# Kernel tuning notes

Measured on AMD Instinct MI355X. Metric: run time of the kernel, lower is better.

Reference implementation:

```python
import jax, jax.numpy as jnp
import numpy as np

N_NODES = 50000
N_EDGES = 600000
N_GRAPHS = 64
D_FEAT = 128
DIM_H = 128
N_HOPS = 3
OUT_DIM = 10


def setup_inputs() -> dict:
    key = jax.random.key(0)
    ks = jax.random.split(key, 16)
    x = jax.random.normal(ks[0], (N_NODES, D_FEAT), dtype=jnp.float32)
    edge_index = jax.random.randint(ks[1], (2, N_EDGES), 0, N_NODES, dtype=jnp.int64)
    batch = jnp.sort(jax.random.randint(ks[2], (N_NODES,), 0, N_GRAPHS, dtype=jnp.int64))
    def glorot(k, shape):
        fan = shape[0] + shape[1]
        return jax.random.uniform(k, shape, jnp.float32, -1.0, 1.0) * np.sqrt(6.0 / fan)
    # GCNConv weights stored as [in, out]; Linear weights stored as [in, out]
    W1 = glorot(ks[3], (D_FEAT, DIM_H)); b1 = jnp.zeros((DIM_H,), jnp.float32)
    W2 = glorot(ks[4], (DIM_H, DIM_H)); b2 = jnp.zeros((DIM_H,), jnp.float32)
    W3 = glorot(ks[5], (DIM_H, DIM_H)); b3 = jnp.zeros((DIM_H,), jnp.float32)
    H3 = DIM_H * N_HOPS
    lin1_W = glorot(ks[6], (H3, H3)); lin1_b = jnp.zeros((H3,), jnp.float32)
    lin2_W = glorot(ks[7], (H3, OUT_DIM)); lin2_b = jnp.zeros((OUT_DIM,), jnp.float32)
    return {"x": x, "W1": W1, "b1": b1, "W2": W2, "b2": b2, "W3": W3, "b3": b3,
            "lin1_W": lin1_W, "lin1_b": lin1_b, "lin2_W": lin2_W, "lin2_b": lin2_b,
            "edge_index": edge_index, "batch": batch}


def gcn_conv(x, W, b, src, dst, n_nodes):
    # PyG GCNConv (add_self_loops=True, normalize=True):
    #   deg[i] = in-degree at target + 1 (self loop); norm = d^-1/2[src] * d^-1/2[dst]
    deg = jnp.zeros((n_nodes,), x.dtype).at[dst].add(1.0) + 1.0
    dinv = jax.lax.rsqrt(deg)
    xw = x @ W  # [N, H] transform before propagate
    coef = (dinv[src] * dinv[dst])[:, None]
    agg = jnp.zeros_like(xw).at[dst].add(xw[src] * coef)
    agg = agg + xw * (dinv * dinv)[:, None]  # self-loop messages
    return agg + b


def global_mean_pool(h, batch, n_graphs):
    sums = jax.ops.segment_sum(h, batch, num_segments=n_graphs)
    cnt = jax.ops.segment_sum(jnp.ones((h.shape[0],), h.dtype), batch, num_segments=n_graphs)
    return sums / jnp.maximum(cnt, 1.0)[:, None]


def reference(x, W1, b1, W2, b2, W3, b3, lin1_W, lin1_b, lin2_W, lin2_b, edge_index, batch):
    src, dst = edge_index[0], edge_index[1]
    n = x.shape[0]
    h1 = gcn_conv(x, W1, b1, src, dst, n)
    h2 = gcn_conv(h1, W2, b2, src, dst, n)
    h3 = gcn_conv(h2, W3, b3, src, dst, n)
    pooled = jnp.concatenate([global_mean_pool(h, batch, N_GRAPHS) for h in (h1, h2, h3)], axis=1)
    h = jax.nn.relu(pooled @ lin1_W + lin1_b)
    # dropout is identity in eval mode
    h = h @ lin2_W + lin2_b
    return (h, jax.nn.log_softmax(h, axis=1))
```

## Files before the change

### kernel.cpp

```cpp
#include <hip/hip_runtime.h>
#include <hip/hip_fp16.h>
#include <math.h>

#define N_NODES 50000
#define N_EDGES 600000
#define N_GRAPHS 64
#define DFEAT 128
#define H3 384
#define OUTD 10
#define SCAN_BLOCKS 196
#define FILL_BLOCKS 2344
#define POOL_CHUNKS 16
#define APAD 136

typedef _Float16 f16x8 __attribute__((ext_vector_type(8)));
typedef float f32x4 __attribute__((ext_vector_type(4)));
typedef float f32x2 __attribute__((ext_vector_type(2)));

__global__ __launch_bounds__(256) void k_deg(const int* __restrict__ ei, int* __restrict__ deg,
                                             int* __restrict__ rank) {
    int e = blockIdx.x * 256 + threadIdx.x;
    if (e >= N_EDGES) return;
    int dst = ei[N_EDGES + e];
    rank[e] = atomicAdd(&deg[dst], 1);
}

__global__ __launch_bounds__(256) void k_part(const int* __restrict__ deg, int* __restrict__ part) {
    __shared__ int red[256];
    int tid = threadIdx.x;
    int i = blockIdx.x * 256 + tid;
    red[tid] = (i < N_NODES) ? deg[i] : 0;
    __syncthreads();
    for (int s = 128; s > 0; s >>= 1) {
        if (tid < s) red[tid] += red[tid + s];
        __syncthreads();
    }
    if (tid == 0) part[blockIdx.x] = red[0];
}

__global__ __launch_bounds__(256) void k_scanpart(const int* __restrict__ part, int* __restrict__ base) {
    __shared__ int buf[256];
    int tid = threadIdx.x;
    int v = (tid < SCAN_BLOCKS) ? part[tid] : 0;
    buf[tid] = v;
    __syncthreads();
    for (int d = 1; d < 256; d <<= 1) {
        int t = (tid >= d) ? buf[tid - d] : 0;
        __syncthreads();
        buf[tid] += t;
        __syncthreads();
    }
    if (tid < SCAN_BLOCKS) base[tid] = buf[tid] - v;
}

__global__ __launch_bounds__(256) void k_offsets(const int* __restrict__ deg, const int* __restrict__ base,
                                                 int* __restrict__ offs, float* __restrict__ dinv) {
    __shared__ int buf[256];
    int tid = threadIdx.x;
    int i = blockIdx.x * 256 + tid;
    int v = (i < N_NODES) ? deg[i] : 0;
    buf[tid] = v;
    __syncthreads();
    for (int d = 1; d < 256; d <<= 1) {
        int t = (tid >= d) ? buf[tid - d] : 0;
        __syncthreads();
        buf[tid] += t;
        __syncthreads();
    }
    if (i < N_NODES) {
        int excl = base[blockIdx.x] + buf[tid] - v;
        offs[i] = excl;
        dinv[i] = rsqrtf((float)v + 1.0f);
        if (i == N_NODES - 1) offs[N_NODES] = base[blockIdx.x] + buf[tid];
    }
}

__global__ __launch_bounds__(256) void k_fill_prep(const int* __restrict__ ei, const int* __restrict__ offs,
                                                   const int* __restrict__ rank, const float* __restrict__ dinv,
                                                   unsigned int* __restrict__ epack,
                                                   const float* __restrict__ W1, const float* __restrict__ W2,
                                                   const float* __restrict__ W3, _Float16* __restrict__ Wt,
                                                   float* __restrict__ pooled) {
    int b = blockIdx.x;
    if (b < FILL_BLOCKS) {
        int e = b * 256 + threadIdx.x;
        if (e >= N_EDGES) return;
        int s = ei[e];
        int t = ei[N_EDGES + e];
        unsigned short dh = __half_as_ushort(__float2half(dinv[s]));
        epack[offs[t] + rank[e]] = (unsigned int)s | ((unsigned int)dh << 16);
    } else if (b < FILL_BLOCKS + 192) {
        int idx = (b - FILL_BLOCKS) * 256 + threadIdx.x;
        int l = idx >> 14, r = idx & 16383;
        const float* W = (l == 0) ? W1 : (l == 1) ? W2 : W3;
        int k = r >> 7, n = r & 127;
        Wt[l * 16384 + n * 128 + k] = (_Float16)W[k * 128 + n];
    } else {
        int idx = (b - FILL_BLOCKS - 192) * 256 + threadIdx.x;
        if (idx < N_GRAPHS * H3) pooled[idx] = 0.0f;
    }
}

template <bool A_FP16>
__global__ __launch_bounds__(256) void gemm_mfma(const void* __restrict__ Aptr, const _Float16* __restrict__ Wt,
                                                 unsigned char* __restrict__ T, int M) {
    __shared__ _Float16 Ws[128 * APAD];
    int tid = threadIdx.x;
    int base = blockIdx.x * 64;
    for (int c = tid; c < 2048; c += 256) {
        int n = c >> 4, c8 = (c & 15) << 3;
        *(f16x8*)&Ws[n * APAD + c8] = *(const f16x8*)&Wt[n * 128 + c8];
    }
    int wave = tid >> 6, lane = tid & 63;
    int m = lane & 15, quad = lane >> 4;
    int gr = base + wave * 16 + m;
    int grc = (gr < M) ? gr : (M - 1);
    f16x8 areg[4];
    if (A_FP16) {
        const _Float16* A = (const _Float16*)Aptr;
#pragma unroll
        for (int kc = 0; kc < 4; ++kc)
            areg[kc] = *(const f16x8*)&A[(size_t)grc * 128 + kc * 32 + quad * 8];
    } else {
        const float* A = (const float*)Aptr;
#pragma unroll
        for (int kc = 0; kc < 4; ++kc) {
            const float* src = A + (size_t)grc * 128 + kc * 32 + quad * 8;
            float4 v0 = *(const float4*)(src);
            float4 v1 = *(const float4*)(src + 4);
            f16x8 h;
            h[0] = (_Float16)v0.x; h[1] = (_Float16)v0.y; h[2] = (_Float16)v0.z; h[3] = (_Float16)v0.w;
            h[4] = (_Float16)v1.x; h[5] = (_Float16)v1.y; h[6] = (_Float16)v1.z; h[7] = (_Float16)v1.w;
            areg[kc] = h;
        }
    }
    __syncthreads();
    f32x4 acc[8];
#pragma unroll
    for (int ct = 0; ct < 8; ++ct) acc[ct] = (f32x4){0.f, 0.f, 0.f, 0.f};
#pragma unroll
    for (int kc = 0; kc < 4; ++kc) {
#pragma unroll
        for (int ct = 0; ct < 8; ++ct) {
            f16x8 b = *(const f16x8*)&Ws[(ct * 16 + m) * APAD + kc * 32 + quad * 8];
            acc[ct] = __builtin_amdgcn_mfma_f32_16x16x32_f16(b, areg[kc], acc[ct], 0, 0, 0);
        }
    }
    if (gr < M) {
#pragma unroll
        for (int ct = 0; ct < 8; ++ct) {
            int col = ct * 16 + quad * 4;
            int p = __builtin_amdgcn_cvt_pk_fp8_f32(acc[ct][0], acc[ct][1], 0, false);
            p     = __builtin_amdgcn_cvt_pk_fp8_f32(acc[ct][2], acc[ct][3], p, true);
            *(int*)(T + (size_t)gr * 128 + col) = p;
        }
    }
}

__global__ __launch_bounds__(256) void gather_agg(const unsigned int* __restrict__ T32,
                                                  const unsigned int* __restrict__ epack,
                                                  const int* __restrict__ offs,
                                                  const float* __restrict__ dinv, const float* __restrict__ bias,
                                                  __half2* __restrict__ H2) {
    int h = threadIdx.x >> 5;
    int l32 = threadIdx.x & 31;
    int node = blockIdx.x * 8 + h;
    unsigned su = T32[(size_t)node * 32 + l32];
    float di = dinv[node];
    float4 b4 = *(const float4*)(bias + l32 * 4);
    float a0 = 0.f, a1 = 0.f, a2 = 0.f, a3 = 0.f;
    int lo = offs[node], hi = offs[node + 1];
    int hm1 = hi - 1;
    for (int e0 = lo; e0 < hi; e0 += 16) {
        unsigned p[16];
#pragma unroll
        for (int j = 0; j < 16; ++j) p[j] = epack[min(e0 + j, hm1)];
        unsigned u[16];
#pragma unroll
        for (int j = 0; j < 16; ++j) u[j] = T32[(size_t)(p[j] & 0xffffu) * 32 + l32];
#pragma unroll
        for (int j = 0; j < 16; ++j) {
            float c = (e0 + j < hi) ? __half2float(__ushort_as_half((unsigned short)(p[j] >> 16))) : 0.0f;
            f32x2 tl = __builtin_amdgcn_cvt_pk_f32_fp8(u[j], false);
            f32x2 th = __builtin_amdgcn_cvt_pk_f32_fp8(u[j], true);
            a0 += tl.x * c; a1 += tl.y * c; a2 += th.x * c; a3 += th.y * c;
        }
    }
    f32x2 sl = __builtin_amdgcn_cvt_pk_f32_fp8(su, false), sh = __builtin_amdgcn_cvt_pk_f32_fp8(su, true);
    float dd = di * di;
    float r0 = di * a0 + sl.x * dd + b4.x;
    float r1 = di * a1 + sl.y * dd + b4.y;
    float r2 = di * a2 + sh.x * dd + b4.z;
    float r3 = di * a3 + sh.y * dd + b4.w;
    H2[(size_t)node * 64 + l32 * 2]     = __floats2half2_rn(r0, r1);
    H2[(size_t)node * 64 + l32 * 2 + 1] = __floats2half2_rn(r2, r3);
}

__global__ __launch_bounds__(256) void pool_kernel(const __half2* __restrict__ H0,
                                                   const __half2* __restrict__ H1,
                                                   const __half2* __restrict__ H2buf,
                                                   const int* __restrict__ batch,
                                                   float* __restrict__ pooled) {
    __shared__ int bounds[2];
    __shared__ float2 red[256];
    int g = blockIdx.x >> 4;
    int chunk = blockIdx.x & (POOL_CHUNKS - 1);
    int tid = threadIdx.x;
    int d2 = tid & 63, sub = tid >> 6;
    if (tid < 2) {
        int target = g + tid;
        int lo = 0, hi = N_NODES;
        while (lo < hi) {
            int mid = (lo + hi) >> 1;
            if (batch[mid] < target) lo = mid + 1; else hi = mid;
        }
        bounds[tid] = lo;
    }
    __syncthreads();
    int lo = bounds[0], hi = bounds[1];
    int n = hi - lo;
    int per = (n + POOL_CHUNKS - 1) / POOL_CHUNKS;
    int s = lo + chunk * per;
    int e = s + per; if (e > hi) e = hi;
    const __half2* Hs[3] = {H0, H1, H2buf};
    for (int l = 0; l < 3; ++l) {
        const __half2* H = Hs[l];
        float ax = 0.0f, ay = 0.0f;
        for (int r = s + sub; r < e; r += 4) {
            float2 v = __half22float2(H[(size_t)r * 64 + d2]);
            ax += v.x; ay += v.y;
        }
        red[tid] = make_float2(ax, ay);
        __syncthreads();
        if (sub == 0 && s < e) {
            float2 v0 = red[d2], v1 = red[64 + d2], v2 = red[128 + d2], v3 = red[192 + d2];
            atomicAdd(&pooled[g * H3 + l * 128 + d2 * 2],     v0.x + v1.x + v2.x + v3.x);
            atomicAdd(&pooled[g * H3 + l * 128 + d2 * 2 + 1], v0.y + v1.y + v2.y + v3.y);
        }
        __syncthreads();
    }
}

__global__ __launch_bounds__(384) void mlp_kernel(const float* __restrict__ pooled,
                                                  const int* __restrict__ batch,
                                                  const float* __restrict__ l1W, const float* __restrict__ l1b,
                                                  const float* __restrict__ l2W, const float* __restrict__ l2b,
                                                  float* __restrict__ out) {
    __shared__ float p[H3];
    __shared__ float hid[H3];
    __shared__ float o10[OUTD];
    __shared__ int bnd[2];
    int g = blockIdx.x, tid = threadIdx.x;
    if (tid < 2) {
        int target = g + tid;
        int lo = 0, hi = N_NODES;
        while (lo < hi) {
            int mid = (lo + hi) >> 1;
            if (batch[mid] < target) lo = mid + 1; else hi = mid;
        }
        bnd[tid] = lo;
    }
    __syncthreads();
    float inv = 1.0f / fmaxf((float)(bnd[1] - bnd[0]), 1.0f);
    p[tid] = pooled[g * H3 + tid] * inv;
    __syncthreads();
    float acc = l1b[tid];
    for (int k = 0; k < H3; ++k) acc += p[k] * l1W[k * H3 + tid];
    hid[tid] = fmaxf(acc, 0.0f);
    __syncthreads();
    if (tid < OUTD) {
        float o = l2b[tid];
        for (int k = 0; k < H3; ++k) o += hid[k] * l2W[k * OUTD + tid];
        o10[tid] = o;
        out[g * OUTD + tid] = o;
    }
    __syncthreads();
    if (tid == 0) {
        float m = o10[0];
        for (int j = 1; j < OUTD; ++j) m = fmaxf(m, o10[j]);
        float s = 0.0f;
        for (int j = 0; j < OUTD; ++j) s += expf(o10[j] - m);
        float lse = m + logf(s);
        for (int j = 0; j < OUTD; ++j) out[N_GRAPHS * OUTD + g * OUTD + j] = o10[j] - lse;
    }
}

extern "C" void kernel_launch(void* const* d_in, const int* in_sizes, int n_in,
                              void* d_out, int out_size, void* d_ws, size_t ws_size,
                              hipStream_t stream) {
    const float* x      = (const float*)d_in[0];
    const float* W1     = (const float*)d_in[1];
    const float* b1     = (const float*)d_in[2];
    const float* W2     = (const float*)d_in[3];
    const float* b2     = (const float*)d_in[4];
    const float* W3     = (const float*)d_in[5];
    const float* b3     = (const float*)d_in[6];
    const float* lin1_W = (const float*)d_in[7];
    const float* lin1_b = (const float*)d_in[8];
    const float* lin2_W = (const float*)d_in[9];
    const float* lin2_b = (const float*)d_in[10];
    const int* edge_index = (const int*)d_in[11];
    const int* batch      = (const int*)d_in[12];

    char* ws = (char*)d_ws;
    auto alloc = [&](size_t bytes) -> void* {
        void* p = (void*)ws;
        ws += (bytes + 255) & ~(size_t)255;
        return p;
    };
    int*   deg    = (int*)  alloc((size_t)N_NODES * 4);
    int*   part   = (int*)  alloc((size_t)SCAN_BLOCKS * 4);
    int*   pbase  = (int*)  alloc((size_t)SCAN_BLOCKS * 4);
    int*   offs   = (int*)  alloc((size_t)(N_NODES + 1) * 4);
    int*   rank   = (int*)  alloc((size_t)N_EDGES * 4);
    float* dinv   = (float*)alloc((size_t)N_NODES * 4);
    unsigned int* epack = (unsigned int*)alloc((size_t)N_EDGES * 4);
    unsigned char* T = (unsigned char*)alloc((size_t)N_NODES * 128);
    __half* Hbuf[3];
    for (int l = 0; l < 3; ++l) Hbuf[l] = (__half*)alloc((size_t)N_NODES * 128 * 2);
    _Float16* Wt  = (_Float16*)alloc((size_t)3 * 128 * 128 * 2);
    float* pooled = (float*)alloc((size_t)N_GRAPHS * H3 * 4);

    hipMemsetAsync(deg, 0, (size_t)N_NODES * 4, stream);
    k_deg<<<(N_EDGES + 255) / 256, 256, 0, stream>>>(edge_index, deg, rank);
    k_part<<<SCAN_BLOCKS, 256, 0, stream>>>(deg, part);
    k_scanpart<<<1, 256, 0, stream>>>(part, pbase);
    k_offsets<<<SCAN_BLOCKS, 256, 0, stream>>>(deg, pbase, offs, dinv);
    k_fill_prep<<<FILL_BLOCKS + 192 + 96, 256, 0, stream>>>(edge_index, offs, rank, dinv, epack,
                                                            W1, W2, W3, Wt, pooled);

    const float* bs[3] = {b1, b2, b3};
    for (int l = 0; l < 3; ++l) {
        if (l == 0)
            gemm_mfma<false><<<(N_NODES + 63) / 64, 256, 0, stream>>>(x, Wt, T, N_NODES);
        else
            gemm_mfma<true><<<(N_NODES + 63) / 64, 256, 0, stream>>>(Hbuf[l - 1], Wt + (size_t)l * 16384, T, N_NODES);
        gather_agg<<<N_NODES / 8, 256, 0, stream>>>((const unsigned int*)T, epack, offs, dinv, bs[l], (__half2*)Hbuf[l]);
    }
    pool_kernel<<<N_GRAPHS * POOL_CHUNKS, 256, 0, stream>>>((const __half2*)Hbuf[0], (const __half2*)Hbuf[1],
                                                            (const __half2*)Hbuf[2], batch, pooled);
    mlp_kernel<<<N_GRAPHS, 384, 0, stream>>>(pooled, batch, lin1_W, lin1_b, lin2_W, lin2_b, (float*)d_out);
}
```

Baseline: 271.3 us.

## Use one 64-lane wave per node in gather and fold partial scan into offsets

```diff
diff --git a/kernel.cpp b/kernel.cpp
--- a/kernel.cpp
+++ b/kernel.cpp
@@ -38,25 +38,21 @@
     if (tid == 0) part[blockIdx.x] = red[0];
 }
 
-__global__ __launch_bounds__(256) void k_scanpart(const int* __restrict__ part, int* __restrict__ base) {
+__global__ __launch_bounds__(256) void k_offsets(const int* __restrict__ deg, const int* __restrict__ part,
+                                                 int* __restrict__ offs, float* __restrict__ dinv) {
+    __shared__ int pbuf[256];
     __shared__ int buf[256];
     int tid = threadIdx.x;
-    int v = (tid < SCAN_BLOCKS) ? part[tid] : 0;
-    buf[tid] = v;
+    int pv = (tid < SCAN_BLOCKS) ? part[tid] : 0;
+    pbuf[tid] = pv;
     __syncthreads();
     for (int d = 1; d < 256; d <<= 1) {
-        int t = (tid >= d) ? buf[tid - d] : 0;
-        __syncthreads();
-        buf[tid] += t;
-        __syncthreads();
-    }
-    if (tid < SCAN_BLOCKS) base[tid] = buf[tid] - v;
-}
-
-__global__ __launch_bounds__(256) void k_offsets(const int* __restrict__ deg, const int* __restrict__ base,
-                                                 int* __restrict__ offs, float* __restrict__ dinv) {
-    __shared__ int buf[256];
-    int tid = threadIdx.x;
+        int t = (tid >= d) ? pbuf[tid - d] : 0;
+        __syncthreads();
+        pbuf[tid] += t;
+        __syncthreads();
+    }
+    int base = (blockIdx.x > 0) ? pbuf[blockIdx.x - 1] : 0;
     int i = blockIdx.x * 256 + tid;
     int v = (i < N_NODES) ? deg[i] : 0;
     buf[tid] = v;
@@ -68,10 +64,10 @@
         __syncthreads();
     }
     if (i < N_NODES) {
-        int excl = base[blockIdx.x] + buf[tid] - v;
+        int excl = base + buf[tid] - v;
         offs[i] = excl;
         dinv[i] = rsqrtf((float)v + 1.0f);
-        if (i == N_NODES - 1) offs[N_NODES] = base[blockIdx.x] + buf[tid];
+        if (i == N_NODES - 1) offs[N_NODES] = base + buf[tid];
     }
 }
 
@@ -157,18 +153,18 @@
     }
 }
 
-__global__ __launch_bounds__(256) void gather_agg(const unsigned int* __restrict__ T32,
+__global__ __launch_bounds__(256) void gather_agg(const unsigned short* __restrict__ T16,
                                                   const unsigned int* __restrict__ epack,
                                                   const int* __restrict__ offs,
                                                   const float* __restrict__ dinv, const float* __restrict__ bias,
                                                   __half2* __restrict__ H2) {
-    int h = threadIdx.x >> 5;
-    int l32 = threadIdx.x & 31;
-    int node = blockIdx.x * 8 + h;
-    unsigned su = T32[(size_t)node * 32 + l32];
+    int w = threadIdx.x >> 6;
+    int l64 = threadIdx.x & 63;
+    int node = blockIdx.x * 4 + w;
+    unsigned su = T16[(size_t)node * 64 + l64];
     float di = dinv[node];
-    float4 b4 = *(const float4*)(bias + l32 * 4);
-    float a0 = 0.f, a1 = 0.f, a2 = 0.f, a3 = 0.f;
+    float2 b2 = *(const float2*)(bias + l64 * 2);
+    float a0 = 0.f, a1 = 0.f;
     int lo = offs[node], hi = offs[node + 1];
     int hm1 = hi - 1;
     for (int e0 = lo; e0 < hi; e0 += 16) {
@@ -177,23 +173,19 @@
         for (int j = 0; j < 16; ++j) p[j] = epack[min(e0 + j, hm1)];
         unsigned u[16];
 #pragma unroll
-        for (int j = 0; j < 16; ++j) u[j] = T32[(size_t)(p[j] & 0xffffu) * 32 + l32];
+        for (int j = 0; j < 16; ++j) u[j] = T16[(size_t)(p[j] & 0xffffu) * 64 + l64];
 #pragma unroll
         for (int j = 0; j < 16; ++j) {
             float c = (e0 + j < hi) ? __half2float(__ushort_as_half((unsigned short)(p[j] >> 16))) : 0.0f;
             f32x2 tl = __builtin_amdgcn_cvt_pk_f32_fp8(u[j], false);
-            f32x2 th = __builtin_amdgcn_cvt_pk_f32_fp8(u[j], true);
-            a0 += tl.x * c; a1 += tl.y * c; a2 += th.x * c; a3 += th.y * c;
-        }
-    }
-    f32x2 sl = __builtin_amdgcn_cvt_pk_f32_fp8(su, false), sh = __builtin_amdgcn_cvt_pk_f32_fp8(su, true);
+            a0 += tl.x * c; a1 += tl.y * c;
+        }
+    }
+    f32x2 sl = __builtin_amdgcn_cvt_pk_f32_fp8(su, false);
     float dd = di * di;
-    float r0 = di * a0 + sl.x * dd + b4.x;
-    float r1 = di * a1 + sl.y * dd + b4.y;
-    float r2 = di * a2 + sh.x * dd + b4.z;
-    float r3 = di * a3 + sh.y * dd + b4.w;
-    H2[(size_t)node * 64 + l32 * 2]     = __floats2half2_rn(r0, r1);
-    H2[(size_t)node * 64 + l32 * 2 + 1] = __floats2half2_rn(r2, r3);
+    float r0 = di * a0 + sl.x * dd + b2.x;
+    float r1 = di * a1 + sl.y * dd + b2.y;
+    H2[(size_t)node * 64 + l64] = __floats2half2_rn(r0, r1);
 }
 
 __global__ __launch_bounds__(256) void pool_kernel(const __half2* __restrict__ H0,
@@ -310,7 +302,6 @@
     };
     int*   deg    = (int*)  alloc((size_t)N_NODES * 4);
     int*   part   = (int*)  alloc((size_t)SCAN_BLOCKS * 4);
-    int*   pbase  = (int*)  alloc((size_t)SCAN_BLOCKS * 4);
     int*   offs   = (int*)  alloc((size_t)(N_NODES + 1) * 4);
     int*   rank   = (int*)  alloc((size_t)N_EDGES * 4);
     float* dinv   = (float*)alloc((size_t)N_NODES * 4);
@@ -324,8 +315,7 @@
     hipMemsetAsync(deg, 0, (size_t)N_NODES * 4, stream);
     k_deg<<<(N_EDGES + 255) / 256, 256, 0, stream>>>(edge_index, deg, rank);
     k_part<<<SCAN_BLOCKS, 256, 0, stream>>>(deg, part);
-    k_scanpart<<<1, 256, 0, stream>>>(part, pbase);
-    k_offsets<<<SCAN_BLOCKS, 256, 0, stream>>>(deg, pbase, offs, dinv);
+    k_offsets<<<SCAN_BLOCKS, 256, 0, stream>>>(deg, part, offs, dinv);
     k_fill_prep<<<FILL_BLOCKS + 192 + 96, 256, 0, stream>>>(edge_index, offs, rank, dinv, epack,
                                                             W1, W2, W3, Wt, pooled);
 
@@ -335,7 +325,7 @@
             gemm_mfma<false><<<(N_NODES + 63) / 64, 256, 0, stream>>>(x, Wt, T, N_NODES);
         else
             gemm_mfma<true><<<(N_NODES + 63) / 64, 256, 0, stream>>>(Hbuf[l - 1], Wt + (size_t)l * 16384, T, N_NODES);
-        gather_agg<<<N_NODES / 8, 256, 0, stream>>>((const unsigned int*)T, epack, offs, dinv, bs[l], (__half2*)Hbuf[l]);
+        gather_agg<<<N_NODES / 4, 256, 0, stream>>>((const unsigned short*)T, epack, offs, dinv, bs[l], (__half2*)Hbuf[l]);
     }
     pool_kernel<<<N_GRAPHS * POOL_CHUNKS, 256, 0, stream>>>((const __half2*)Hbuf[0], (const __half2*)Hbuf[1],
                                                             (const __half2*)Hbuf[2], batch, pooled);
```

Measured after the change: 293.5 us. +8.2%, slower.
